# Kernel optimization log

Measured on AMD Instinct MI355X. Metric: run time of the kernel, lower is better.

The kernel has to match this reference:

```python
import jax, jax.numpy as jnp
import numpy as np

N_GRIDS, N_FEATS = 64, 2
GD = GH = GW = 64
PE_TERMS, N_DIMS = 6, 3
NODES, N_OUT = 64, 1
N_PTS = 524288


def setup_inputs() -> dict:
    key = jax.random.key(0)
    ks = jax.random.split(key, 8)
    x = jax.random.uniform(ks[0], (N_PTS, N_DIMS), jnp.float32, -1.0, 1.0)
    grid_scales = jax.random.uniform(ks[1], (N_GRIDS, 3), jnp.float32, 1.0, 4.0)
    grid_translations = jax.random.uniform(ks[2], (N_GRIDS, 3), jnp.float32, -1.0, 1.0) * (grid_scales - 1.0)
    feature_grids = jax.random.normal(ks[3], (N_GRIDS, N_FEATS, GD, GH, GW), jnp.float32)
    d_in = PE_TERMS * N_DIMS * 2 + N_FEATS * N_GRIDS  # 36 + 128 = 164
    W0 = jax.random.normal(ks[4], (d_in, NODES), jnp.float32) * np.sqrt(2.0 / (d_in + NODES))
    b0 = jnp.zeros((NODES,), jnp.float32)
    W1 = jax.random.normal(ks[5], (NODES, NODES), jnp.float32) * np.sqrt(2.0 / (2 * NODES))
    b1 = jnp.zeros((NODES,), jnp.float32)
    W2 = jax.random.normal(ks[6], (NODES, N_OUT), jnp.float32) * np.sqrt(2.0 / (NODES + N_OUT))
    b2 = jnp.zeros((N_OUT,), jnp.float32)
    return dict(x=x, grid_scales=grid_scales, grid_translations=grid_translations,
                feature_grids=feature_grids, W0=W0, b0=b0, W1=W1, b1=b1, W2=W2, b2=b2)


def grid_sample_3d(vol, coords):
    """Trilinear grid_sample, align_corners=True, padding_mode='zeros'.
    vol: [C,D,H,W]; coords: [N,3] in (x,y,z) order (x -> W axis), range [-1,1].
    Returns [C,N]."""
    C, D, H, W = vol.shape
    flat = vol.reshape(C, D * H * W)
    ix = (coords[:, 0] + 1.0) * 0.5 * (W - 1)
    iy = (coords[:, 1] + 1.0) * 0.5 * (H - 1)
    iz = (coords[:, 2] + 1.0) * 0.5 * (D - 1)
    x0 = jnp.floor(ix); y0 = jnp.floor(iy); z0 = jnp.floor(iz)
    wx = ix - x0; wy = iy - y0; wz = iz - z0
    x0i = x0.astype(jnp.int32); y0i = y0.astype(jnp.int32); z0i = z0.astype(jnp.int32)
    out = jnp.zeros((C, coords.shape[0]), vol.dtype)
    for dz, wz_ in ((0, 1.0 - wz), (1, wz)):
        for dy, wy_ in ((0, 1.0 - wy), (1, wy)):
            for dx, wx_ in ((0, 1.0 - wx), (1, wx)):
                xi = x0i + dx; yi = y0i + dy; zi = z0i + dz
                valid = (xi >= 0) & (xi < W) & (yi >= 0) & (yi < H) & (zi >= 0) & (zi < D)
                idx = (jnp.clip(zi, 0, D - 1) * H + jnp.clip(yi, 0, H - 1)) * W + jnp.clip(xi, 0, W - 1)
                v = jnp.take(flat, idx, axis=1) * valid.astype(vol.dtype)[None, :]
                out = out + v * (wz_ * wy_ * wx_)[None, :]
    return out


def positional_encoding(x):
    # NeRF-style PE: sin/cos of pi*2^i * x, i in [0, PE_TERMS), out dim = 2*L*3
    freqs = jnp.pi * (2.0 ** jnp.arange(PE_TERMS, dtype=jnp.float32))  # [L]
    ang = x[:, None, :] * freqs[None, :, None]                          # [N,L,3]
    n = x.shape[0]
    return jnp.concatenate([jnp.sin(ang).reshape(n, -1), jnp.cos(ang).reshape(n, -1)], axis=1)


def snake_alt(x):
    return 0.5 * x + jnp.sin(x) ** 2


def reference(x, grid_scales, grid_translations, feature_grids, W0, b0, W1, b1, W2, b2):
    # per-grid affine transform (equivalent to bmm with the scale+translation 4x4)
    tp = x[None, :, :] * grid_scales[:, None, :] + grid_translations[:, None, :]  # [G,N,3]
    feats = jax.vmap(grid_sample_3d)(feature_grids, tp)  # [G,C,N]
    G, C, N = feats.shape
    feats = feats.reshape(G * C, N).T                    # [N, G*C]
    pe = positional_encoding(x)                          # [N, 2*L*3]
    y = jnp.concatenate([pe, feats], axis=1)
    y = snake_alt(y @ W0 + b0)
    y = snake_alt(y @ W1 + b1)
    y = y @ W2 + b2
    return y
```

## Files before the change

kernel.cpp:

```cpp
#include <hip/hip_runtime.h>
#include <hip/hip_bf16.h>

#define NPTS    524288
#define NG      64
#define GSZ     64
#define VOX     (GSZ*GSZ*GSZ)
#define NODES   64
#define TILE    64
#define NBLK    (NPTS / TILE)
#define K0      192
#define SF      200
#define NCELL   4096
#define PREP_VB 16384
#define PREP_CB 2048

typedef __attribute__((ext_vector_type(8))) short bf16x8;
typedef __attribute__((ext_vector_type(4))) float f32x4;

__device__ inline unsigned short f2bf(float f) {
    __hip_bfloat16 b = __float2bfloat16(f);
    union { __hip_bfloat16 h; unsigned short u; } cv; cv.h = b;
    return cv.u;
}
__device__ inline unsigned int pk2(float c0, float c1) {
    return (unsigned int)f2bf(c0) | ((unsigned int)f2bf(c1) << 16);
}
__device__ inline float bflo(unsigned int v) { return __uint_as_float(v << 16); }
__device__ inline float bfhi(unsigned int v) { return __uint_as_float(v & 0xffff0000u); }

__device__ inline int spread4(int v) {
    return (v & 1) | ((v & 2) << 2) | ((v & 4) << 4) | ((v & 8) << 6);
}
__device__ inline int cell_of(float px, float py, float pz) {
    int cx = min(max((int)((px + 1.0f) * 8.0f), 0), 15);
    int cy = min(max((int)((py + 1.0f) * 8.0f), 0), 15);
    int cz = min(max((int)((pz + 1.0f) * 8.0f), 0), 15);
    return spread4(cx) | (spread4(cy) << 1) | (spread4(cz) << 2);
}


__global__ void prep_fused(const float* __restrict__ fg, uint4* __restrict__ vox4,
                           const float* __restrict__ x, unsigned short* __restrict__ cid,
                           int* __restrict__ hist,
                           const float* __restrict__ W0, const float* __restrict__ W1,
                           unsigned short* __restrict__ w0t, unsigned short* __restrict__ w1t) {
    int b = blockIdx.x;
    int tid = threadIdx.x;
    if (b < PREP_VB) {
        int idx = b * 256 + tid;
        int g = idx >> 16;
        int hb = idx & 65535;
        int brick = hb >> 1;
        int h = hb & 1;
        int bx = brick & 31, by = (brick >> 5) & 31, bz = brick >> 10;
        int xx = bx << 1, yy = by << 1, zz = (bz << 1) + h;
        const float* c0 = fg + (size_t)g * (2 * VOX) + ((zz << 6) + yy) * 64 + xx;
        const float* c1 = c0 + VOX;
        float2 a0 = *(const float2*)c0;
        float2 a1 = *(const float2*)(c0 + 64);
        float2 d0 = *(const float2*)c1;
        float2 d1 = *(const float2*)(c1 + 64);
        vox4[idx] = make_uint4(pk2(a0.x, d0.x), pk2(a0.y, d0.y),
                               pk2(a1.x, d1.x), pk2(a1.y, d1.y));
    } else if (b < PREP_VB + PREP_CB) {
        int p = (b - PREP_VB) * 256 + tid;
        int c = cell_of(x[p * 3 + 0], x[p * 3 + 1], x[p * 3 + 2]);
        cid[p] = (unsigned short)c;
        atomicAdd(&hist[c], 1);
    } else {
        int t = (b - PREP_VB - PREP_CB) * 256 + tid;
        for (int i = t; i < NODES * K0; i += 4096) {
            int n = i / K0, k = i - n * K0;
            w0t[i] = (k < 164) ? f2bf(W0[k * NODES + n]) : (unsigned short)0;
        }
        for (int i = t; i < NODES * NODES; i += 4096) {
            int n = i >> 6, k = i & 63;
            w1t[i] = f2bf(W1[k * NODES + n]);
        }
    }
}

__global__ void sort_scan(const int* __restrict__ hist, int* __restrict__ offs) {
    __shared__ int partial[256];
    int t = threadIdx.x;
    int loc[16];
    int s = 0;
    #pragma unroll
    for (int i = 0; i < 16; ++i) { loc[i] = s; s += hist[t * 16 + i]; }
    partial[t] = s;
    __syncthreads();
    for (int d = 1; d < 256; d <<= 1) {
        int v = (t >= d) ? partial[t - d] : 0;
        __syncthreads();
        partial[t] += v;
        __syncthreads();
    }
    int base = partial[t] - s;
    #pragma unroll
    for (int i = 0; i < 16; ++i) offs[t * 16 + i] = base + loc[i];
}

__global__ void sort_scatter(const float* __restrict__ x, const unsigned short* __restrict__ cell_id,
                             int* __restrict__ offs, float4* __restrict__ spts) {
    int p = blockIdx.x * blockDim.x + threadIdx.x;
    int c = cell_id[p];
    int pos = atomicAdd(&offs[c], 1);
    spts[pos] = make_float4(x[p * 3 + 0], x[p * 3 + 1], x[p * 3 + 2], __int_as_float(p));
}

__device__ inline void gather_pair(int pt, int g, float ix, float iy, float iz,
                                   const unsigned int* __restrict__ vox,
                                   unsigned short* Fsh) {
    float fx = floorf(ix), fy = floorf(iy), fz = floorf(iz);
    int x0 = (int)fx, y0 = (int)fy, z0 = (int)fz;
    float wx = ix - fx, wy = iy - fy, wz = iz - fz;
    float wxa0 = (x0 >= 0) ? (1.0f - wx) : 0.0f;
    float wxa1 = (x0 < 63) ? wx : 0.0f;
    float wya0 = (y0 >= 0) ? (1.0f - wy) : 0.0f;
    float wya1 = (y0 < 63) ? wy : 0.0f;
    float wza0 = (z0 >= 0) ? (1.0f - wz) : 0.0f;
    float wza1 = (z0 < 63) ? wz : 0.0f;
    int xc0 = max(x0, 0), xc1 = min(x0 + 1, 63);
    int yc0 = max(y0, 0), yc1 = min(y0 + 1, 63);
    int zc0 = max(z0, 0), zc1 = min(z0 + 1, 63);
    int xp0 = ((xc0 >> 1) << 3) | (xc0 & 1);
    int xp1 = ((xc1 >> 1) << 3) | (xc1 & 1);
    int yp0 = ((yc0 >> 1) << 8) | ((yc0 & 1) << 1);
    int yp1 = ((yc1 >> 1) << 8) | ((yc1 & 1) << 1);
    int zp0 = ((zc0 >> 1) << 13) | ((zc0 & 1) << 2);
    int zp1 = ((zc1 >> 1) << 13) | ((zc1 & 1) << 2);
    const unsigned int* vg = vox + ((size_t)g << 18);
    float f0 = 0.f, f1 = 0.f;
    #pragma unroll
    for (int dz = 0; dz < 2; ++dz) {
        int zp = dz ? zp1 : zp0; float wzv = dz ? wza1 : wza0;
        #pragma unroll
        for (int dy = 0; dy < 2; ++dy) {
            int rowb = zp + (dy ? yp1 : yp0);
            float wzy = wzv * (dy ? wya1 : wya0);
            unsigned int v0 = vg[rowb + xp0], v1 = vg[rowb + xp1];
            f0 += wzy * (wxa0 * bflo(v0) + wxa1 * bflo(v1));
            f1 += wzy * (wxa0 * bfhi(v0) + wxa1 * bfhi(v1));
        }
    }
    *(unsigned int*)&Fsh[pt * SF + 36 + 2 * g] = pk2(f0, f1);
}

__global__ void __launch_bounds__(256, 5)
amrsrn_main(const float4* __restrict__ spts,
            const float* __restrict__ gscale,
            const float* __restrict__ gtrans,
            const unsigned int* __restrict__ vox,
            const unsigned short* __restrict__ w0t,
            const unsigned short* __restrict__ w1t,
            const float* __restrict__ b0,
            const float* __restrict__ b1,
            const float* __restrict__ W2,
            const float* __restrict__ b2,
            float* __restrict__ out) {
    __shared__ unsigned short Fsh[TILE * SF];
    __shared__ int   sidx[TILE];
    __shared__ float gss[NG * 3];
    __shared__ float gts[NG * 3];

    const int tid = threadIdx.x;
    const int lane = tid & 63;
    const int wv = tid >> 6;
    const int cb = ((blockIdx.x & 7) << 10) | (blockIdx.x >> 3);
    const int base = cb * TILE;

    for (int i = tid; i < TILE * SF / 8; i += 256) ((uint4*)Fsh)[i] = make_uint4(0,0,0,0);
    float4 sp = spts[base + lane];
    const float px = sp.x, py = sp.y, pz = sp.z;
    if (tid < TILE) sidx[tid] = __float_as_int(sp.w);
    if (tid < NG * 3) { gss[tid] = gscale[tid]; gts[tid] = gtrans[tid]; }
    __syncthreads();

    float lox = px, hix = px, loy = py, hiy = py, loz = pz, hiz = pz;
    #pragma unroll
    for (int m = 1; m < 64; m <<= 1) {
        lox = fminf(lox, __shfl_xor(lox, m)); hix = fmaxf(hix, __shfl_xor(hix, m));
        loy = fminf(loy, __shfl_xor(loy, m)); hiy = fmaxf(hiy, __shfl_xor(hiy, m));
        loz = fminf(loz, __shfl_xor(loz, m)); hiz = fmaxf(hiz, __shfl_xor(hiz, m));
    }
    unsigned long long mfull, mpart;
    {
        int g = lane;
        float s0 = gss[g*3+0], s1 = gss[g*3+1], s2 = gss[g*3+2];
        float t0 = gts[g*3+0], t1 = gts[g*3+1], t2 = gts[g*3+2];
        float xl = (lox*s0 + t0 + 1.0f)*31.5f, xh = (hix*s0 + t0 + 1.0f)*31.5f;
        float yl = (loy*s1 + t1 + 1.0f)*31.5f, yh = (hiy*s1 + t1 + 1.0f)*31.5f;
        float zl = (loz*s2 + t2 + 1.0f)*31.5f, zh = (hiz*s2 + t2 + 1.0f)*31.5f;
        bool fullg = (xl >= -0.999f) & (xh <= 63.999f)
                   & (yl >= -0.999f) & (yh <= 63.999f)
                   & (zl >= -0.999f) & (zh <= 63.999f);
        bool outg  = (xh < -1.001f) | (xl >= 64.001f)
                   | (yh < -1.001f) | (yl >= 64.001f)
                   | (zh < -1.001f) | (zl >= 64.001f);
        mfull = __ballot(fullg);
        mpart = __ballot(!fullg && !outg);
    }

    {
        #pragma unroll
        for (int t = 0; t < 9; ++t) {
            int tau = wv * 9 + t;
            int tt = (tau < 18) ? tau : tau - 18;
            int l = tt / 3, d = tt - l * 3;
            float c = (d == 0) ? px : ((d == 1) ? py : pz);
            float ang = c * (3.14159265358979323846f * (float)(1 << l));
            float val = (tau < 18) ? __sinf(ang) : __cosf(ang);
            Fsh[lane * SF + tau] = f2bf(val);
        }
    }

    {
        int idx = 0;
        unsigned long long m = mfull;
        while (m) {
            int g = __builtin_ctzll(m);
            m &= m - 1;
            if ((idx++ & 3) == wv) {
                float ix = (px * gss[g*3+0] + gts[g*3+0] + 1.0f) * 31.5f;
                float iy = (py * gss[g*3+1] + gts[g*3+1] + 1.0f) * 31.5f;
                float iz = (pz * gss[g*3+2] + gts[g*3+2] + 1.0f) * 31.5f;
                gather_pair(lane, g, ix, iy, iz, vox, Fsh);
            }
        }
        m = mpart;
        while (m) {
            int g = __builtin_ctzll(m);
            m &= m - 1;
            if ((idx++ & 3) == wv) {
                float ix = (px * gss[g*3+0] + gts[g*3+0] + 1.0f) * 31.5f;
                float iy = (py * gss[g*3+1] + gts[g*3+1] + 1.0f) * 31.5f;
                float iz = (pz * gss[g*3+2] + gts[g*3+2] + 1.0f) * 31.5f;
                bool valid = (ix >= -1.0f) & (ix < 64.0f)
                           & (iy >= -1.0f) & (iy < 64.0f)
                           & (iz >= -1.0f) & (iz < 64.0f);
                if (valid) gather_pair(lane, g, ix, iy, iz, vox, Fsh);
            }
        }
    }
    __syncthreads();

    const int ptb = wv * 16;
    const int row = lane & 15;
    const int quad = lane >> 4;
    const int koff = quad * 8;

    f32x4 acc0[4] = {{0,0,0,0},{0,0,0,0},{0,0,0,0},{0,0,0,0}};
    #pragma unroll
    for (int ks = 0; ks < 6; ++ks) {
        bf16x8 a = *(const bf16x8*)&Fsh[(ptb + row) * SF + ks * 32 + koff];
        #pragma unroll
        for (int nt = 0; nt < 4; ++nt) {
            bf16x8 b = *(const bf16x8*)&w0t[(nt * 16 + row) * K0 + ks * 32 + koff];
            acc0[nt] = __builtin_amdgcn_mfma_f32_16x16x32_bf16(a, b, acc0[nt], 0, 0, 0);
        }
    }
    #pragma unroll
    for (int nt = 0; nt < 4; ++nt) {
        int node = nt * 16 + row;
        float bb = b0[node];
        #pragma unroll
        for (int r = 0; r < 4; ++r) {
            float h = acc0[nt][r] + bb;
            float s = __sinf(h);
            h = 0.5f * h + s * s;
            Fsh[(ptb + quad * 4 + r) * SF + node] = f2bf(h);
        }
    }

    f32x4 acc1[4] = {{0,0,0,0},{0,0,0,0},{0,0,0,0},{0,0,0,0}};
    #pragma unroll
    for (int ks = 0; ks < 2; ++ks) {
        bf16x8 a = *(const bf16x8*)&Fsh[(ptb + row) * SF + ks * 32 + koff];
        #pragma unroll
        for (int nt = 0; nt < 4; ++nt) {
            bf16x8 b = *(const bf16x8*)&w1t[(nt * 16 + row) * NODES + ks * 32 + koff];
            acc1[nt] = __builtin_amdgcn_mfma_f32_16x16x32_bf16(a, b, acc1[nt], 0, 0, 0);
        }
    }
    float part[4] = {0.f, 0.f, 0.f, 0.f};
    #pragma unroll
    for (int nt = 0; nt < 4; ++nt) {
        int node = nt * 16 + row;
        float b1v = b1[node];
        float w2v = W2[node];
        #pragma unroll
        for (int r = 0; r < 4; ++r) {
            float h = acc1[nt][r] + b1v;
            float s = __sinf(h);
            h = 0.5f * h + s * s;
            part[r] += h * w2v;
        }
    }
    #pragma unroll
    for (int m = 1; m < 16; m <<= 1) {
        #pragma unroll
        for (int r = 0; r < 4; ++r) part[r] += __shfl_xor(part[r], m);
    }
    if (row == 0) {
        float b2v = b2[0];
        #pragma unroll
        for (int r = 0; r < 4; ++r) {
            int pt = ptb + quad * 4 + r;
            out[sidx[pt]] = part[r] + b2v;
        }
    }
}

__global__ void amrsrn_fallback(const float* __restrict__ x,
                                const float* __restrict__ gscale,
                                const float* __restrict__ gtrans,
                                const float* __restrict__ fg,
                                const float* __restrict__ W0,
                                const float* __restrict__ b0,
                                const float* __restrict__ W1,
                                const float* __restrict__ b1,
                                const float* __restrict__ W2,
                                const float* __restrict__ b2,
                                float* __restrict__ out) {
    int p = blockIdx.x * blockDim.x + threadIdx.x;
    float px = x[p*3+0], py = x[p*3+1], pz = x[p*3+2];
    float h0[NODES];
    #pragma unroll
    for (int j = 0; j < NODES; ++j) h0[j] = b0[j];
    #pragma unroll
    for (int l = 0; l < 6; ++l) {
        float freq = 3.14159265358979323846f * (float)(1 << l);
        #pragma unroll
        for (int d = 0; d < 3; ++d) {
            float v = (d == 0 ? px : (d == 1 ? py : pz)) * freq;
            float s = __sinf(v), c = __cosf(v);
            const float* wrs = W0 + (l*3 + d) * NODES;
            const float* wrc = W0 + (18 + l*3 + d) * NODES;
            #pragma unroll
            for (int j = 0; j < NODES; ++j) h0[j] += s * wrs[j] + c * wrc[j];
        }
    }
    for (int g = 0; g < NG; ++g) {
        float ix = (px * gscale[g*3+0] + gtrans[g*3+0] + 1.0f) * 31.5f;
        float iy = (py * gscale[g*3+1] + gtrans[g*3+1] + 1.0f) * 31.5f;
        float iz = (pz * gscale[g*3+2] + gtrans[g*3+2] + 1.0f) * 31.5f;
        float fxf = floorf(ix), fyf = floorf(iy), fzf = floorf(iz);
        int x0 = (int)fxf, y0 = (int)fyf, z0 = (int)fzf;
        float wx = ix - fxf, wy = iy - fyf, wz = iz - fzf;
        bool any = (x0 >= -1 && x0 < GSZ) && (y0 >= -1 && y0 < GSZ) && (z0 >= -1 && z0 < GSZ);
        if (any) {
            float f0 = 0.f, f1 = 0.f;
            #pragma unroll
            for (int dz = 0; dz < 2; ++dz) {
                int zi = z0 + dz; bool vz = ((unsigned)zi < (unsigned)GSZ);
                int zc = min(max(zi, 0), GSZ - 1);
                float wzf = dz ? wz : 1.f - wz;
                #pragma unroll
                for (int dy = 0; dy < 2; ++dy) {
                    int yi = y0 + dy; bool vy = ((unsigned)yi < (unsigned)GSZ);
                    int yc = min(max(yi, 0), GSZ - 1);
                    float wyf = dy ? wy : 1.f - wy;
                    int rowoff = (zc * GSZ + yc) * GSZ;
                    #pragma unroll
                    for (int dx = 0; dx < 2; ++dx) {
                        int xi = x0 + dx; bool vx = ((unsigned)xi < (unsigned)GSZ);
                        int xc = min(max(xi, 0), GSZ - 1);
                        float w = wzf * wyf * (dx ? wx : 1.f - wx);
                        w = (vz && vy && vx) ? w : 0.f;
                        const float* gp = fg + ((size_t)g << 19);
                        f0 += w * gp[rowoff + xc];
                        f1 += w * gp[VOX + rowoff + xc];
                    }
                }
            }
            const float* wr = W0 + (36 + 2*g) * NODES;
            #pragma unroll
            for (int j = 0; j < NODES; ++j) h0[j] += f0 * wr[j] + f1 * wr[NODES + j];
        }
    }
    #pragma unroll
    for (int j = 0; j < NODES; ++j) { float s = __sinf(h0[j]); h0[j] = 0.5f * h0[j] + s * s; }
    float out_acc = b2[0];
    #pragma unroll
    for (int half = 0; half < 2; ++half) {
        float h1[32];
        #pragma unroll
        for (int j = 0; j < 32; ++j) h1[j] = b1[half*32 + j];
        #pragma unroll
        for (int i = 0; i < NODES; ++i) {
            float a = h0[i];
            const float* w1r = W1 + i * NODES + half*32;
            #pragma unroll
            for (int j = 0; j < 32; ++j) h1[j] += a * w1r[j];
        }
        #pragma unroll
        for (int j = 0; j < 32; ++j) { float s = __sinf(h1[j]); out_acc += (0.5f * h1[j] + s * s) * W2[half*32 + j]; }
    }
    out[p] = out_acc;
}

extern "C" void kernel_launch(void* const* d_in, const int* in_sizes, int n_in,
                              void* d_out, int out_size, void* d_ws, size_t ws_size,
                              hipStream_t stream) {
    const float* x      = (const float*)d_in[0];
    const float* gscale = (const float*)d_in[1];
    const float* gtrans = (const float*)d_in[2];
    const float* fg     = (const float*)d_in[3];
    const float* W0     = (const float*)d_in[4];
    const float* b0     = (const float*)d_in[5];
    const float* W1     = (const float*)d_in[6];
    const float* b1     = (const float*)d_in[7];
    const float* W2     = (const float*)d_in[8];
    const float* b2     = (const float*)d_in[9];
    float* out = (float*)d_out;

    char* wsp = (char*)d_ws;
    unsigned short* w0t = (unsigned short*)wsp;
    unsigned short* w1t = w0t + NODES * K0;
    int* hist           = (int*)(wsp + (64 << 10));
    int* offs           = (int*)(wsp + (80 << 10));
    unsigned short* cid = (unsigned short*)(wsp + (96 << 10));
    float4* spts        = (float4*)(wsp + (96 << 10) + (1 << 20));
    unsigned int* vox   = (unsigned int*)(wsp + (96 << 10) + (1 << 20) + (8 << 20));
    const size_t ws_needed = (96 << 10) + (1 << 20) + (8 << 20) + (size_t)NG * VOX * 4;

    if (ws_size >= ws_needed) {
        hipMemsetAsync(hist, 0, NCELL * sizeof(int), stream);
        prep_fused<<<PREP_VB + PREP_CB + 16, 256, 0, stream>>>(
            fg, (uint4*)vox, x, cid, hist, W0, W1, w0t, w1t);
        sort_scan<<<1, 256, 0, stream>>>(hist, offs);
        sort_scatter<<<NPTS / 256, 256, 0, stream>>>(x, cid, offs, spts);
        amrsrn_main<<<NBLK, 256, 0, stream>>>(spts, gscale, gtrans, vox,
                                              w0t, w1t, b0, b1, W2, b2, out);
    } else {
        amrsrn_fallback<<<NPTS / 256, 256, 0, stream>>>(
            x, gscale, gtrans, fg, W0, b0, W1, b1, W2, b2, out);
    }
}
```

Measured before the change: 448.4 us.

## Batch two grid gathers per wave and regroup block-to-cell mapping

The per-grid trilinear gather is restructured so each wave issues the 16 voxel loads for two grids before doing any arithmetic. This raises memory-level parallelism and hides more gather latency, at the cost of extra registers under launch bounds of 5 blocks per SM. Partial-grid samples that fall outside the volume are still loaded but not written. The block-index swizzle also changes, so neighbouring blocks now map to cells in 32-block chunks rather than striding 1024 apart, which affects L2 locality across concurrent blocks.

```diff
diff --git a/kernel.cpp b/kernel.cpp
--- a/kernel.cpp
+++ b/kernel.cpp
@@ -108,42 +108,106 @@
     spts[pos] = make_float4(x[p * 3 + 0], x[p * 3 + 1], x[p * 3 + 2], __int_as_float(p));
 }
 
-__device__ inline void gather_pair(int pt, int g, float ix, float iy, float iz,
-                                   const unsigned int* __restrict__ vox,
-                                   unsigned short* Fsh) {
+struct GP {
+    int xp0, xp1, yp0, yp1, zp0, zp1;
+    float wx0, wx1, wy0, wy1, wz0, wz1;
+    const unsigned int* vg;
+};
+__device__ inline GP gprep(int g, float ix, float iy, float iz,
+                           const unsigned int* __restrict__ vox) {
+    GP p;
     float fx = floorf(ix), fy = floorf(iy), fz = floorf(iz);
     int x0 = (int)fx, y0 = (int)fy, z0 = (int)fz;
     float wx = ix - fx, wy = iy - fy, wz = iz - fz;
-    float wxa0 = (x0 >= 0) ? (1.0f - wx) : 0.0f;
-    float wxa1 = (x0 < 63) ? wx : 0.0f;
-    float wya0 = (y0 >= 0) ? (1.0f - wy) : 0.0f;
-    float wya1 = (y0 < 63) ? wy : 0.0f;
-    float wza0 = (z0 >= 0) ? (1.0f - wz) : 0.0f;
-    float wza1 = (z0 < 63) ? wz : 0.0f;
+    p.wx0 = (x0 >= 0) ? (1.0f - wx) : 0.0f;
+    p.wx1 = (x0 < 63) ? wx : 0.0f;
+    p.wy0 = (y0 >= 0) ? (1.0f - wy) : 0.0f;
+    p.wy1 = (y0 < 63) ? wy : 0.0f;
+    p.wz0 = (z0 >= 0) ? (1.0f - wz) : 0.0f;
+    p.wz1 = (z0 < 63) ? wz : 0.0f;
     int xc0 = max(x0, 0), xc1 = min(x0 + 1, 63);
     int yc0 = max(y0, 0), yc1 = min(y0 + 1, 63);
     int zc0 = max(z0, 0), zc1 = min(z0 + 1, 63);
-    int xp0 = ((xc0 >> 1) << 3) | (xc0 & 1);
-    int xp1 = ((xc1 >> 1) << 3) | (xc1 & 1);
-    int yp0 = ((yc0 >> 1) << 8) | ((yc0 & 1) << 1);
-    int yp1 = ((yc1 >> 1) << 8) | ((yc1 & 1) << 1);
-    int zp0 = ((zc0 >> 1) << 13) | ((zc0 & 1) << 2);
-    int zp1 = ((zc1 >> 1) << 13) | ((zc1 & 1) << 2);
-    const unsigned int* vg = vox + ((size_t)g << 18);
-    float f0 = 0.f, f1 = 0.f;
-    #pragma unroll
-    for (int dz = 0; dz < 2; ++dz) {
-        int zp = dz ? zp1 : zp0; float wzv = dz ? wza1 : wza0;
-        #pragma unroll
-        for (int dy = 0; dy < 2; ++dy) {
-            int rowb = zp + (dy ? yp1 : yp0);
-            float wzy = wzv * (dy ? wya1 : wya0);
-            unsigned int v0 = vg[rowb + xp0], v1 = vg[rowb + xp1];
-            f0 += wzy * (wxa0 * bflo(v0) + wxa1 * bflo(v1));
-            f1 += wzy * (wxa0 * bfhi(v0) + wxa1 * bfhi(v1));
-        }
-    }
-    *(unsigned int*)&Fsh[pt * SF + 36 + 2 * g] = pk2(f0, f1);
+    p.xp0 = ((xc0 >> 1) << 3) | (xc0 & 1);
+    p.xp1 = ((xc1 >> 1) << 3) | (xc1 & 1);
+    p.yp0 = ((yc0 >> 1) << 8) | ((yc0 & 1) << 1);
+    p.yp1 = ((yc1 >> 1) << 8) | ((yc1 & 1) << 1);
+    p.zp0 = ((zc0 >> 1) << 13) | ((zc0 & 1) << 2);
+    p.zp1 = ((zc1 >> 1) << 13) | ((zc1 & 1) << 2);
+    p.vg = vox + ((size_t)g << 18);
+    return p;
+}
+
+__device__ inline void gather2(int pt, int gA, float axi, float ayi, float azi, bool wrA,
+                               int gB, float bxi, float byi, float bzi, bool wrB,
+                               const unsigned int* __restrict__ vox,
+                               unsigned short* Fsh) {
+    GP a = gprep(gA, axi, ayi, azi, vox);
+    GP b = gprep(gB, bxi, byi, bzi, vox);
+    unsigned int a00 = a.vg[a.zp0 + a.yp0 + a.xp0], a01 = a.vg[a.zp0 + a.yp0 + a.xp1];
+    unsigned int a10 = a.vg[a.zp0 + a.yp1 + a.xp0], a11 = a.vg[a.zp0 + a.yp1 + a.xp1];
+    unsigned int a20 = a.vg[a.zp1 + a.yp0 + a.xp0], a21 = a.vg[a.zp1 + a.yp0 + a.xp1];
+    unsigned int a30 = a.vg[a.zp1 + a.yp1 + a.xp0], a31 = a.vg[a.zp1 + a.yp1 + a.xp1];
+    unsigned int b00 = b.vg[b.zp0 + b.yp0 + b.xp0], b01 = b.vg[b.zp0 + b.yp0 + b.xp1];
+    unsigned int b10 = b.vg[b.zp0 + b.yp1 + b.xp0], b11 = b.vg[b.zp0 + b.yp1 + b.xp1];
+    unsigned int b20 = b.vg[b.zp1 + b.yp0 + b.xp0], b21 = b.vg[b.zp1 + b.yp0 + b.xp1];
+    unsigned int b30 = b.vg[b.zp1 + b.yp1 + b.xp0], b31 = b.vg[b.zp1 + b.yp1 + b.xp1];
+    {
+        float f0 = 0.f, f1 = 0.f, wzy;
+        wzy = a.wz0 * a.wy0;
+        f0 += wzy * (a.wx0 * bflo(a00) + a.wx1 * bflo(a01));
+        f1 += wzy * (a.wx0 * bfhi(a00) + a.wx1 * bfhi(a01));
+        wzy = a.wz0 * a.wy1;
+        f0 += wzy * (a.wx0 * bflo(a10) + a.wx1 * bflo(a11));
+        f1 += wzy * (a.wx0 * bfhi(a10) + a.wx1 * bfhi(a11));
+        wzy = a.wz1 * a.wy0;
+        f0 += wzy * (a.wx0 * bflo(a20) + a.wx1 * bflo(a21));
+        f1 += wzy * (a.wx0 * bfhi(a20) + a.wx1 * bfhi(a21));
+        wzy = a.wz1 * a.wy1;
+        f0 += wzy * (a.wx0 * bflo(a30) + a.wx1 * bflo(a31));
+        f1 += wzy * (a.wx0 * bfhi(a30) + a.wx1 * bfhi(a31));
+        if (wrA) *(unsigned int*)&Fsh[pt * SF + 36 + 2 * gA] = pk2(f0, f1);
+    }
+    {
+        float f0 = 0.f, f1 = 0.f, wzy;
+        wzy = b.wz0 * b.wy0;
+        f0 += wzy * (b.wx0 * bflo(b00) + b.wx1 * bflo(b01));
+        f1 += wzy * (b.wx0 * bfhi(b00) + b.wx1 * bfhi(b01));
+        wzy = b.wz0 * b.wy1;
+        f0 += wzy * (b.wx0 * bflo(b10) + b.wx1 * bflo(b11));
+        f1 += wzy * (b.wx0 * bfhi(b10) + b.wx1 * bfhi(b11));
+        wzy = b.wz1 * b.wy0;
+        f0 += wzy * (b.wx0 * bflo(b20) + b.wx1 * bflo(b21));
+        f1 += wzy * (b.wx0 * bfhi(b20) + b.wx1 * bfhi(b21));
+        wzy = b.wz1 * b.wy1;
+        f0 += wzy * (b.wx0 * bflo(b30) + b.wx1 * bflo(b31));
+        f1 += wzy * (b.wx0 * bfhi(b30) + b.wx1 * bfhi(b31));
+        if (wrB) *(unsigned int*)&Fsh[pt * SF + 36 + 2 * gB] = pk2(f0, f1);
+    }
+}
+
+__device__ inline void gather1(int pt, int g, float ix, float iy, float iz, bool wr,
+                               const unsigned int* __restrict__ vox,
+                               unsigned short* Fsh) {
+    GP a = gprep(g, ix, iy, iz, vox);
+    unsigned int a00 = a.vg[a.zp0 + a.yp0 + a.xp0], a01 = a.vg[a.zp0 + a.yp0 + a.xp1];
+    unsigned int a10 = a.vg[a.zp0 + a.yp1 + a.xp0], a11 = a.vg[a.zp0 + a.yp1 + a.xp1];
+    unsigned int a20 = a.vg[a.zp1 + a.yp0 + a.xp0], a21 = a.vg[a.zp1 + a.yp0 + a.xp1];
+    unsigned int a30 = a.vg[a.zp1 + a.yp1 + a.xp0], a31 = a.vg[a.zp1 + a.yp1 + a.xp1];
+    float f0 = 0.f, f1 = 0.f, wzy;
+    wzy = a.wz0 * a.wy0;
+    f0 += wzy * (a.wx0 * bflo(a00) + a.wx1 * bflo(a01));
+    f1 += wzy * (a.wx0 * bfhi(a00) + a.wx1 * bfhi(a01));
+    wzy = a.wz0 * a.wy1;
+    f0 += wzy * (a.wx0 * bflo(a10) + a.wx1 * bflo(a11));
+    f1 += wzy * (a.wx0 * bfhi(a10) + a.wx1 * bfhi(a11));
+    wzy = a.wz1 * a.wy0;
+    f0 += wzy * (a.wx0 * bflo(a20) + a.wx1 * bflo(a21));
+    f1 += wzy * (a.wx0 * bfhi(a20) + a.wx1 * bfhi(a21));
+    wzy = a.wz1 * a.wy1;
+    f0 += wzy * (a.wx0 * bflo(a30) + a.wx1 * bflo(a31));
+    f1 += wzy * (a.wx0 * bfhi(a30) + a.wx1 * bfhi(a31));
+    if (wr) *(unsigned int*)&Fsh[pt * SF + 36 + 2 * g] = pk2(f0, f1);
 }
 
 __global__ void __launch_bounds__(256, 5)
@@ -166,7 +230,7 @@
     const int tid = threadIdx.x;
     const int lane = tid & 63;
     const int wv = tid >> 6;
-    const int cb = ((blockIdx.x & 7) << 10) | (blockIdx.x >> 3);
+    const int cb = ((blockIdx.x >> 8) << 8) | ((blockIdx.x & 7) << 5) | ((blockIdx.x >> 3) & 31);
     const int base = cb * TILE;
 
     for (int i = tid; i < TILE * SF / 8; i += 256) ((uint4*)Fsh)[i] = make_uint4(0,0,0,0);
@@ -216,31 +280,31 @@
 
     {
         int idx = 0;
-        unsigned long long m = mfull;
-        while (m) {
-            int g = __builtin_ctzll(m);
-            m &= m - 1;
-            if ((idx++ & 3) == wv) {
+        int gq = -1; float qx = 0.f, qy = 0.f, qz = 0.f; bool qw = false;
+        #pragma unroll 1
+        for (int pass = 0; pass < 2; ++pass) {
+            unsigned long long m = pass ? mpart : mfull;
+            while (m) {
+                int g = __builtin_ctzll(m);
+                m &= m - 1;
+                if ((idx++ & 3) != wv) continue;
                 float ix = (px * gss[g*3+0] + gts[g*3+0] + 1.0f) * 31.5f;
                 float iy = (py * gss[g*3+1] + gts[g*3+1] + 1.0f) * 31.5f;
                 float iz = (pz * gss[g*3+2] + gts[g*3+2] + 1.0f) * 31.5f;
-                gather_pair(lane, g, ix, iy, iz, vox, Fsh);
+                bool wr = true;
+                if (pass) {
+                    wr = (ix >= -1.0f) & (ix < 64.0f)
+                       & (iy >= -1.0f) & (iy < 64.0f)
+                       & (iz >= -1.0f) & (iz < 64.0f);
+                }
+                if (gq < 0) { gq = g; qx = ix; qy = iy; qz = iz; qw = wr; }
+                else {
+                    gather2(lane, gq, qx, qy, qz, qw, g, ix, iy, iz, wr, vox, Fsh);
+                    gq = -1;
+                }
             }
         }
-        m = mpart;
-        while (m) {
-            int g = __builtin_ctzll(m);
-            m &= m - 1;
-            if ((idx++ & 3) == wv) {
-                float ix = (px * gss[g*3+0] + gts[g*3+0] + 1.0f) * 31.5f;
-                float iy = (py * gss[g*3+1] + gts[g*3+1] + 1.0f) * 31.5f;
-                float iz = (pz * gss[g*3+2] + gts[g*3+2] + 1.0f) * 31.5f;
-                bool valid = (ix >= -1.0f) & (ix < 64.0f)
-                           & (iy >= -1.0f) & (iy < 64.0f)
-                           & (iz >= -1.0f) & (iz < 64.0f);
-                if (valid) gather_pair(lane, g, ix, iy, iz, vox, Fsh);
-            }
-        }
+        if (gq >= 0) gather1(lane, gq, qx, qy, qz, qw, vox, Fsh);
     }
     __syncthreads();
 
```

Result: no change. 448.1 us (-0.1%).
